# Performance work log

Hardware: AMD Instinct MI355X
Metric: run time of the kernel (lower is better)

Reference implementation:

```python
import jax, jax.numpy as jnp
import numpy as np

EPS = 1e-8  # torch cosine_similarity eps


def setup_inputs() -> dict:
    key = jax.random.key(0)
    kq, km = jax.random.split(key)
    B, N, D = 256, 100000, 1024
    query = jax.random.normal(kq, (B, D), dtype=jnp.float32)
    memory = jax.random.normal(km, (N, D), dtype=jnp.float32)
    return {"query": query, "memory": memory, "k": 16}


def reference(query, memory, k):
    # Batched, fused version of HierarchicalMemory.retrieve():
    # cosine similarity of each query against every stored module, then top-k.
    # sim(q, m) = q.m / max(||q||*||m||, eps), matching F.cosine_similarity.
    qn = jnp.linalg.norm(query, axis=-1)          # [B]
    mn = jnp.linalg.norm(memory, axis=-1)         # [N]
    dots = jnp.einsum("bd,nd->bn", query, memory)  # [B, N]
    sims = dots / jnp.maximum(qn[:, None] * mn[None, :], EPS)
    top_vals, top_idx = jax.lax.top_k(sims, k)    # [B, k] each
    return top_vals, top_idx
```

## Files before the change

### kernel.cpp

```cpp
#include <hip/hip_runtime.h>
#include <math.h>

#define DDIM 1024
#define BQ 256
#define EPSV 1e-8f
#define CH 4
#define TPC 32
#define NCAND (CH * TPC)

typedef short bf16x8 __attribute__((ext_vector_type(8)));
typedef float f32x4 __attribute__((ext_vector_type(4)));

__device__ __forceinline__ unsigned short f2bf(float x) {
  union { float f; unsigned int u; } v;
  v.f = x;
  unsigned int lsb = (v.u >> 16) & 1u;
  v.u += 0x7fffu + lsb;
  return (unsigned short)(v.u >> 16);
}
__device__ __forceinline__ float bf2f(unsigned short b) {
  union { unsigned int u; float f; } v;
  v.u = ((unsigned int)b) << 16;
  return v.f;
}

#define ASYNC_CP16(gp, lp)                                                     \
  __builtin_amdgcn_global_load_lds(                                            \
      (const __attribute__((address_space(1))) unsigned int*)(const void*)(gp),\
      (__attribute__((address_space(3))) unsigned int*)(lp), 16, 0, 0)

__global__ __launch_bounds__(256) void prep_q(const float* __restrict__ Q,
                                              unsigned short* __restrict__ Qb,
                                              float* __restrict__ qn) {
  int wave = threadIdx.x >> 6, lane = threadIdx.x & 63;
  int q = blockIdx.x * 4 + wave;
  const float4* src = (const float4*)(Q + (size_t)q * DDIM);
  unsigned short* dst = Qb + (size_t)q * DDIM;
  float s = 0.f;
#pragma unroll
  for (int t = 0; t < 4; ++t) {
    float4 v = src[t * 64 + lane];
    s += v.x * v.x + v.y * v.y + v.z * v.z + v.w * v.w;
    ushort4 o;
    o.x = f2bf(v.x); o.y = f2bf(v.y); o.z = f2bf(v.z); o.w = f2bf(v.w);
    *(ushort4*)(dst + t * 256 + lane * 4) = o;
  }
#pragma unroll
  for (int o = 32; o > 0; o >>= 1) s += __shfl_down(s, o, 64);
  if (lane == 0) qn[q] = sqrtf(s);
}

__global__ __launch_bounds__(256) void gemm_topk(
    const float* __restrict__ M, const unsigned short* __restrict__ Qb,
    unsigned short* __restrict__ sims, float* __restrict__ rmn,
    int N, int Npitch) {
  __shared__ unsigned short Qs[256 * 32];
  __shared__ unsigned short Ms[64 * 32];
  const int tid = threadIdx.x;
  const int wave = tid >> 6, lane = tid & 63;
  const int quad = lane >> 4, l15 = lane & 15;
  const int n0 = blockIdx.x * 64;

  const int mrow = tid >> 2;
  const int mchunk = tid & 3;
  const bool mvalid = (n0 + mrow) < N;
  const float* mptr = M + (size_t)(mvalid ? (n0 + mrow) : 0) * DDIM + mchunk * 8;

  f32x4 acc[4][4];
#pragma unroll
  for (int i = 0; i < 4; ++i)
#pragma unroll
    for (int j = 0; j < 4; ++j) acc[i][j] = (f32x4){0.f, 0.f, 0.f, 0.f};
  float sumsq = 0.f;

  for (int k0 = 0; k0 < DDIM; k0 += 32) {
    float4 m0, m1;
    if (mvalid) {
      m0 = *(const float4*)(mptr + k0);
      m1 = *(const float4*)(mptr + k0 + 4);
    } else {
      m0 = make_float4(0.f, 0.f, 0.f, 0.f);
      m1 = m0;
    }
    __syncthreads();
#pragma unroll
    for (int r = 0; r < 4; ++r) {
      int row0 = r * 64 + wave * 16;
      const unsigned short* g =
          Qb + (size_t)(row0 + (lane >> 2)) * DDIM + k0 + (lane & 3) * 8;
      ASYNC_CP16(g, &Qs[row0 * 32]);
    }
    sumsq += m0.x * m0.x + m0.y * m0.y + m0.z * m0.z + m0.w * m0.w +
             m1.x * m1.x + m1.y * m1.y + m1.z * m1.z + m1.w * m1.w;
    uint4 packed;
    packed.x = (unsigned int)f2bf(m0.x) | ((unsigned int)f2bf(m0.y) << 16);
    packed.y = (unsigned int)f2bf(m0.z) | ((unsigned int)f2bf(m0.w) << 16);
    packed.z = (unsigned int)f2bf(m1.x) | ((unsigned int)f2bf(m1.y) << 16);
    packed.w = (unsigned int)f2bf(m1.z) | ((unsigned int)f2bf(m1.w) << 16);
    *(uint4*)&Ms[mrow * 32 + mchunk * 8] = packed;
    __syncthreads();
    bf16x8 afr[4], bfr[4];
#pragma unroll
    for (int i = 0; i < 4; ++i)
      afr[i] = *(const bf16x8*)&Qs[(wave * 64 + i * 16 + l15) * 32 + quad * 8];
#pragma unroll
    for (int j = 0; j < 4; ++j)
      bfr[j] = *(const bf16x8*)&Ms[(j * 16 + l15) * 32 + quad * 8];
#pragma unroll
    for (int i = 0; i < 4; ++i)
#pragma unroll
      for (int j = 0; j < 4; ++j)
        acc[i][j] = __builtin_amdgcn_mfma_f32_16x16x32_bf16(afr[i], bfr[j],
                                                            acc[i][j], 0, 0, 0);
  }

  float s = sumsq;
  s += __shfl_xor(s, 1, 64);
  s += __shfl_xor(s, 2, 64);
  if (mchunk == 0) rmn[n0 + mrow] = (s > 0.f) ? rsqrtf(s) : 0.f;

#pragma unroll
  for (int i = 0; i < 4; ++i)
#pragma unroll
    for (int j = 0; j < 4; ++j)
#pragma unroll
      for (int r = 0; r < 4; ++r) {
        int q = wave * 64 + i * 16 + quad * 4 + r;
        int n = n0 + j * 16 + l15;
        sims[(size_t)q * Npitch + n] = f2bf(acc[i][j][r]);
      }
}

__device__ __forceinline__ bool better(float v1, int i1, float v2, int i2) {
  return v1 > v2 || (v1 == v2 && i1 < i2);
}

template <int L>
__device__ __forceinline__ void insert_topL(float (&tv)[L], int (&ti)[L],
                                            float v, int idx) {
  if (v > tv[L - 1] || (v == tv[L - 1] && idx < ti[L - 1])) {
    tv[L - 1] = v; ti[L - 1] = idx;
#pragma unroll
    for (int j = L - 1; j > 0; --j) {
      if (better(tv[j], ti[j], tv[j - 1], ti[j - 1])) {
        float fv = tv[j]; tv[j] = tv[j - 1]; tv[j - 1] = fv;
        int ii = ti[j]; ti[j] = ti[j - 1]; ti[j - 1] = ii;
      }
    }
  }
}

template <int L, typename F>
__device__ __forceinline__ void block_extract(float (&tv)[L], int (&ti)[L],
                                              int rounds, F&& emit) {
  __shared__ float s_v[4];
  __shared__ int s_i[4];
  __shared__ int s_t[4];
  __shared__ float s_wv;
  __shared__ int s_wi;
  __shared__ int s_wt;
  for (int r = 0; r < rounds; ++r) {
    float v = tv[0];
    int idx = ti[0];
    int src = threadIdx.x;
#pragma unroll
    for (int o = 32; o > 0; o >>= 1) {
      float ov = __shfl_down(v, o, 64);
      int oi = __shfl_down(idx, o, 64);
      int os = __shfl_down(src, o, 64);
      if (better(ov, oi, v, idx)) { v = ov; idx = oi; src = os; }
    }
    int lane = threadIdx.x & 63, w = threadIdx.x >> 6;
    if (lane == 0) { s_v[w] = v; s_i[w] = idx; s_t[w] = src; }
    __syncthreads();
    if (threadIdx.x == 0) {
      float bv = s_v[0]; int bi = s_i[0]; int bt = s_t[0];
      for (int w2 = 1; w2 < 4; ++w2)
        if (better(s_v[w2], s_i[w2], bv, bi)) { bv = s_v[w2]; bi = s_i[w2]; bt = s_t[w2]; }
      s_wv = bv; s_wi = bi; s_wt = bt;
    }
    __syncthreads();
    if (threadIdx.x == s_wt) {
#pragma unroll
      for (int j = 0; j < L - 1; ++j) { tv[j] = tv[j + 1]; ti[j] = ti[j + 1]; }
      tv[L - 1] = -INFINITY; ti[L - 1] = 0x7fffffff;
    }
    if (threadIdx.x == 0) emit(r, s_wv, s_wi);
    __syncthreads();
  }
}

__global__ __launch_bounds__(256) void select_chunks(
    const unsigned short* __restrict__ sims, const float* __restrict__ rmn,
    int* __restrict__ cand, int N, int Npitch, int Nc) {
  int q = blockIdx.y;
  int c = blockIdx.x;
  int start = c * Nc;
  int end = start + Nc;
  if (end > N) end = N;
  float tv[8]; int ti[8];
#pragma unroll
  for (int j = 0; j < 8; ++j) { tv[j] = -INFINITY; ti[j] = 0x7fffffff; }
  const unsigned short* row = sims + (size_t)q * Npitch;
  int base = start + threadIdx.x * 8;
  for (; base + 8 <= end; base += 2048) {
    uint4 wv = *(const uint4*)(row + base);
    float4 r0 = *(const float4*)&rmn[base];
    float4 r1 = *(const float4*)&rmn[base + 4];
    float f0 = bf2f((unsigned short)(wv.x & 0xffff)) * r0.x;
    float f1 = bf2f((unsigned short)(wv.x >> 16)) * r0.y;
    float f2 = bf2f((unsigned short)(wv.y & 0xffff)) * r0.z;
    float f3 = bf2f((unsigned short)(wv.y >> 16)) * r0.w;
    float f4 = bf2f((unsigned short)(wv.z & 0xffff)) * r1.x;
    float f5 = bf2f((unsigned short)(wv.z >> 16)) * r1.y;
    float f6 = bf2f((unsigned short)(wv.w & 0xffff)) * r1.z;
    float f7 = bf2f((unsigned short)(wv.w >> 16)) * r1.w;
    insert_topL<8>(tv, ti, f0, base + 0);
    insert_topL<8>(tv, ti, f1, base + 1);
    insert_topL<8>(tv, ti, f2, base + 2);
    insert_topL<8>(tv, ti, f3, base + 3);
    insert_topL<8>(tv, ti, f4, base + 4);
    insert_topL<8>(tv, ti, f5, base + 5);
    insert_topL<8>(tv, ti, f6, base + 6);
    insert_topL<8>(tv, ti, f7, base + 7);
  }
  if (base < end) {
    for (int n = base; n < end; ++n)
      insert_topL<8>(tv, ti, bf2f(row[n]) * rmn[n], n);
  }
  int* dst = cand + (size_t)q * NCAND + c * TPC;
  block_extract<8>(tv, ti, TPC, [&](int r, float v, int i) {
    dst[r] = (i == 0x7fffffff) ? 0 : i;
  });
}

__global__ __launch_bounds__(512) void rescore(
    const float* __restrict__ Q, const float* __restrict__ M,
    const float* __restrict__ qn, const int* __restrict__ cand,
    float* __restrict__ out, int N) {
  __shared__ float cosv[NCAND];
  __shared__ int cidx[NCAND];
  int q = blockIdx.x;
  int wave = threadIdx.x >> 6, lane = threadIdx.x & 63;
  const float4* qf4 = (const float4*)(Q + (size_t)q * DDIM);
  float4 qv[4];
#pragma unroll
  for (int t = 0; t < 4; ++t) qv[t] = qf4[t * 64 + lane];
  float qnv = qn[q];
#pragma unroll 1
  for (int i = 0; i < NCAND / 8; ++i) {
    int c = wave * (NCAND / 8) + i;
    int idx = cand[(size_t)q * NCAND + c];
    if (idx < 0 || idx >= N) idx = 0;
    const float4* mf4 = (const float4*)(M + (size_t)idx * DDIM);
    float dot = 0.f, sq = 0.f;
#pragma unroll
    for (int t = 0; t < 4; ++t) {
      float4 m = mf4[t * 64 + lane];
      dot += m.x * qv[t].x + m.y * qv[t].y + m.z * qv[t].z + m.w * qv[t].w;
      sq += m.x * m.x + m.y * m.y + m.z * m.z + m.w * m.w;
    }
#pragma unroll
    for (int o = 32; o > 0; o >>= 1) {
      dot += __shfl_down(dot, o, 64);
      sq += __shfl_down(sq, o, 64);
    }
    if (lane == 0) {
      cosv[c] = dot / fmaxf(qnv * sqrtf(sq), EPSV);
      cidx[c] = idx;
    }
  }
  __syncthreads();
  if (wave == 0) {
    float v0 = cosv[lane], v1 = cosv[lane + 64];
    int i0 = cidx[lane], i1 = cidx[lane + 64];
    for (int r = 0; r < 16; ++r) {
      bool fb = better(v0, i0, v1, i1);
      float bv = fb ? v0 : v1;
      int bi = fb ? i0 : i1;
      int bs = lane * 2 + (fb ? 0 : 1);
#pragma unroll
      for (int o = 32; o > 0; o >>= 1) {
        float ov = __shfl_down(bv, o, 64);
        int oi = __shfl_down(bi, o, 64);
        int os = __shfl_down(bs, o, 64);
        if (better(ov, oi, bv, bi)) { bv = ov; bi = oi; bs = os; }
      }
      bv = __shfl(bv, 0, 64);
      bi = __shfl(bi, 0, 64);
      bs = __shfl(bs, 0, 64);
      if (lane == (bs >> 1)) {
        if (bs & 1) v1 = -INFINITY; else v0 = -INFINITY;
      }
      if (lane == 0) {
        out[(size_t)q * 16 + r] = bv;
        out[(size_t)BQ * 16 + (size_t)q * 16 + r] = (float)bi;
      }
    }
  }
}

extern "C" void kernel_launch(void* const* d_in, const int* in_sizes, int n_in,
                              void* d_out, int out_size, void* d_ws, size_t ws_size,
                              hipStream_t stream) {
  const float* Q = (const float*)d_in[0];
  const float* M = (const float*)d_in[1];
  int N = in_sizes[1] / DDIM;
  float* out = (float*)d_out;

  int nb = (N + 63) / 64;
  int Npitch = nb * 64;

  char* w = (char*)d_ws;
  size_t off = 0;
  auto alloc = [&](size_t bytes) {
    char* p = w + off;
    off = (off + bytes + 255) & ~(size_t)255;
    return p;
  };
  unsigned short* Qb = (unsigned short*)alloc((size_t)BQ * DDIM * 2);
  float* qn = (float*)alloc((size_t)BQ * 4);
  float* rmn = (float*)alloc((size_t)Npitch * 4);
  int* cand = (int*)alloc((size_t)BQ * NCAND * 4);
  unsigned short* sims = (unsigned short*)alloc((size_t)BQ * Npitch * 2);
  (void)ws_size;

  int Nc = (((N + CH - 1) / CH) + 7) & ~7;

  prep_q<<<BQ / 4, 256, 0, stream>>>(Q, Qb, qn);
  gemm_topk<<<nb, 256, 0, stream>>>(M, Qb, sims, rmn, N, Npitch);
  select_chunks<<<dim3(CH, BQ), 256, 0, stream>>>(sims, rmn, cand, N, Npitch, Nc);
  rescore<<<BQ, 512, 0, stream>>>(Q, M, qn, cand, out, N);
}
```

Before: 745.5 us.

## Fold memory-norm scaling into GEMM epilogue, prefetch M, widen selection and rescore

The GEMM kernel now applies the reciprocal memory-row norm in its epilogue through shared memory, so the rmn buffer and its reads in the selection kernel go away. The fp32 memory loads are software-prefetched one k-step ahead to overlap global latency with MFMA work. Selection uses 8 chunks of 512 threads, each thread keeping a top-16 list, and emits 16 candidates per chunk. Rescoring processes two candidates per iteration to raise memory-level parallelism. The larger per-thread top-16 lists cost more registers and insertion work, and the tail loop in selection is now capped at 8 elements.

```diff
diff --git a/kernel.cpp b/kernel.cpp
--- a/kernel.cpp
+++ b/kernel.cpp
@@ -4,8 +4,8 @@
 #define DDIM 1024
 #define BQ 256
 #define EPSV 1e-8f
-#define CH 4
-#define TPC 32
+#define CH 8
+#define TPC 16
 #define NCAND (CH * TPC)
 
 typedef short bf16x8 __attribute__((ext_vector_type(8)));
@@ -52,10 +52,10 @@
 
 __global__ __launch_bounds__(256) void gemm_topk(
     const float* __restrict__ M, const unsigned short* __restrict__ Qb,
-    unsigned short* __restrict__ sims, float* __restrict__ rmn,
-    int N, int Npitch) {
+    unsigned short* __restrict__ sims, int N, int Npitch) {
   __shared__ unsigned short Qs[256 * 32];
   __shared__ unsigned short Ms[64 * 32];
+  __shared__ float Rs[64];
   const int tid = threadIdx.x;
   const int wave = tid >> 6, lane = tid & 63;
   const int quad = lane >> 4, l15 = lane & 15;
@@ -73,15 +73,13 @@
     for (int j = 0; j < 4; ++j) acc[i][j] = (f32x4){0.f, 0.f, 0.f, 0.f};
   float sumsq = 0.f;
 
+  float4 m0 = make_float4(0.f, 0.f, 0.f, 0.f), m1 = m0;
+  if (mvalid) {
+    m0 = *(const float4*)(mptr);
+    m1 = *(const float4*)(mptr + 4);
+  }
+
   for (int k0 = 0; k0 < DDIM; k0 += 32) {
-    float4 m0, m1;
-    if (mvalid) {
-      m0 = *(const float4*)(mptr + k0);
-      m1 = *(const float4*)(mptr + k0 + 4);
-    } else {
-      m0 = make_float4(0.f, 0.f, 0.f, 0.f);
-      m1 = m0;
-    }
     __syncthreads();
 #pragma unroll
     for (int r = 0; r < 4; ++r) {
@@ -99,6 +97,11 @@
     packed.w = (unsigned int)f2bf(m1.z) | ((unsigned int)f2bf(m1.w) << 16);
     *(uint4*)&Ms[mrow * 32 + mchunk * 8] = packed;
     __syncthreads();
+    float4 m0n = make_float4(0.f, 0.f, 0.f, 0.f), m1n = m0n;
+    if (k0 + 32 < DDIM && mvalid) {
+      m0n = *(const float4*)(mptr + k0 + 32);
+      m1n = *(const float4*)(mptr + k0 + 36);
+    }
     bf16x8 afr[4], bfr[4];
 #pragma unroll
     for (int i = 0; i < 4; ++i)
@@ -112,12 +115,18 @@
       for (int j = 0; j < 4; ++j)
         acc[i][j] = __builtin_amdgcn_mfma_f32_16x16x32_bf16(afr[i], bfr[j],
                                                             acc[i][j], 0, 0, 0);
+    m0 = m0n;
+    m1 = m1n;
   }
 
   float s = sumsq;
   s += __shfl_xor(s, 1, 64);
   s += __shfl_xor(s, 2, 64);
-  if (mchunk == 0) rmn[n0 + mrow] = (s > 0.f) ? rsqrtf(s) : 0.f;
+  if (mchunk == 0) Rs[mrow] = (s > 0.f) ? rsqrtf(s) : 0.f;
+  __syncthreads();
+  float rj[4];
+#pragma unroll
+  for (int j = 0; j < 4; ++j) rj[j] = Rs[j * 16 + l15];
 
 #pragma unroll
   for (int i = 0; i < 4; ++i)
@@ -127,7 +136,7 @@
       for (int r = 0; r < 4; ++r) {
         int q = wave * 64 + i * 16 + quad * 4 + r;
         int n = n0 + j * 16 + l15;
-        sims[(size_t)q * Npitch + n] = f2bf(acc[i][j][r]);
+        sims[(size_t)q * Npitch + n] = f2bf(acc[i][j][r] * rj[j]);
       }
 }
 
@@ -150,12 +159,12 @@
   }
 }
 
-template <int L, typename F>
+template <int L, int NW, typename F>
 __device__ __forceinline__ void block_extract(float (&tv)[L], int (&ti)[L],
                                               int rounds, F&& emit) {
-  __shared__ float s_v[4];
-  __shared__ int s_i[4];
-  __shared__ int s_t[4];
+  __shared__ float s_v[NW];
+  __shared__ int s_i[NW];
+  __shared__ int s_t[NW];
   __shared__ float s_wv;
   __shared__ int s_wi;
   __shared__ int s_wt;
@@ -175,7 +184,7 @@
     __syncthreads();
     if (threadIdx.x == 0) {
       float bv = s_v[0]; int bi = s_i[0]; int bt = s_t[0];
-      for (int w2 = 1; w2 < 4; ++w2)
+      for (int w2 = 1; w2 < NW; ++w2)
         if (better(s_v[w2], s_i[w2], bv, bi)) { bv = s_v[w2]; bi = s_i[w2]; bt = s_t[w2]; }
       s_wv = bv; s_wi = bi; s_wt = bt;
     }
@@ -190,46 +199,45 @@
   }
 }
 
-__global__ __launch_bounds__(256) void select_chunks(
-    const unsigned short* __restrict__ sims, const float* __restrict__ rmn,
-    int* __restrict__ cand, int N, int Npitch, int Nc) {
+__global__ __launch_bounds__(512) void select_chunks(
+    const unsigned short* __restrict__ sims, int* __restrict__ cand,
+    int N, int Npitch, int Nc) {
   int q = blockIdx.y;
   int c = blockIdx.x;
   int start = c * Nc;
   int end = start + Nc;
   if (end > N) end = N;
-  float tv[8]; int ti[8];
-#pragma unroll
-  for (int j = 0; j < 8; ++j) { tv[j] = -INFINITY; ti[j] = 0x7fffffff; }
+  float tv[16]; int ti[16];
+#pragma unroll
+  for (int j = 0; j < 16; ++j) { tv[j] = -INFINITY; ti[j] = 0x7fffffff; }
   const unsigned short* row = sims + (size_t)q * Npitch;
   int base = start + threadIdx.x * 8;
-  for (; base + 8 <= end; base += 2048) {
+  for (; base + 8 <= end; base += 4096) {
     uint4 wv = *(const uint4*)(row + base);
-    float4 r0 = *(const float4*)&rmn[base];
-    float4 r1 = *(const float4*)&rmn[base + 4];
-    float f0 = bf2f((unsigned short)(wv.x & 0xffff)) * r0.x;
-    float f1 = bf2f((unsigned short)(wv.x >> 16)) * r0.y;
-    float f2 = bf2f((unsigned short)(wv.y & 0xffff)) * r0.z;
-    float f3 = bf2f((unsigned short)(wv.y >> 16)) * r0.w;
-    float f4 = bf2f((unsigned short)(wv.z & 0xffff)) * r1.x;
-    float f5 = bf2f((unsigned short)(wv.z >> 16)) * r1.y;
-    float f6 = bf2f((unsigned short)(wv.w & 0xffff)) * r1.z;
-    float f7 = bf2f((unsigned short)(wv.w >> 16)) * r1.w;
-    insert_topL<8>(tv, ti, f0, base + 0);
-    insert_topL<8>(tv, ti, f1, base + 1);
-    insert_topL<8>(tv, ti, f2, base + 2);
-    insert_topL<8>(tv, ti, f3, base + 3);
-    insert_topL<8>(tv, ti, f4, base + 4);
-    insert_topL<8>(tv, ti, f5, base + 5);
-    insert_topL<8>(tv, ti, f6, base + 6);
-    insert_topL<8>(tv, ti, f7, base + 7);
+    float f0 = bf2f((unsigned short)(wv.x & 0xffff));
+    float f1 = bf2f((unsigned short)(wv.x >> 16));
+    float f2 = bf2f((unsigned short)(wv.y & 0xffff));
+    float f3 = bf2f((unsigned short)(wv.y >> 16));
+    float f4 = bf2f((unsigned short)(wv.z & 0xffff));
+    float f5 = bf2f((unsigned short)(wv.z >> 16));
+    float f6 = bf2f((unsigned short)(wv.w & 0xffff));
+    float f7 = bf2f((unsigned short)(wv.w >> 16));
+    insert_topL<16>(tv, ti, f0, base + 0);
+    insert_topL<16>(tv, ti, f1, base + 1);
+    insert_topL<16>(tv, ti, f2, base + 2);
+    insert_topL<16>(tv, ti, f3, base + 3);
+    insert_topL<16>(tv, ti, f4, base + 4);
+    insert_topL<16>(tv, ti, f5, base + 5);
+    insert_topL<16>(tv, ti, f6, base + 6);
+    insert_topL<16>(tv, ti, f7, base + 7);
   }
   if (base < end) {
-    for (int n = base; n < end; ++n)
-      insert_topL<8>(tv, ti, bf2f(row[n]) * rmn[n], n);
+    int stop = end - base < 8 ? end : base + 8;
+    for (int n = base; n < stop; ++n)
+      insert_topL<16>(tv, ti, bf2f(row[n]), n);
   }
   int* dst = cand + (size_t)q * NCAND + c * TPC;
-  block_extract<8>(tv, ti, TPC, [&](int r, float v, int i) {
+  block_extract<16, 8>(tv, ti, TPC, [&](int r, float v, int i) {
     dst[r] = (i == 0x7fffffff) ? 0 : i;
   });
 }
@@ -247,27 +255,39 @@
 #pragma unroll
   for (int t = 0; t < 4; ++t) qv[t] = qf4[t * 64 + lane];
   float qnv = qn[q];
+  const int per = NCAND / 8;
 #pragma unroll 1
-  for (int i = 0; i < NCAND / 8; ++i) {
-    int c = wave * (NCAND / 8) + i;
-    int idx = cand[(size_t)q * NCAND + c];
-    if (idx < 0 || idx >= N) idx = 0;
-    const float4* mf4 = (const float4*)(M + (size_t)idx * DDIM);
-    float dot = 0.f, sq = 0.f;
+  for (int i = 0; i < per; i += 2) {
+    int cA = wave * per + i;
+    int cB = cA + 1;
+    int idxA = cand[(size_t)q * NCAND + cA];
+    int idxB = cand[(size_t)q * NCAND + cB];
+    if (idxA < 0 || idxA >= N) idxA = 0;
+    if (idxB < 0 || idxB >= N) idxB = 0;
+    const float4* mA = (const float4*)(M + (size_t)idxA * DDIM);
+    const float4* mB = (const float4*)(M + (size_t)idxB * DDIM);
+    float dA = 0.f, sA = 0.f, dB = 0.f, sB = 0.f;
 #pragma unroll
     for (int t = 0; t < 4; ++t) {
-      float4 m = mf4[t * 64 + lane];
-      dot += m.x * qv[t].x + m.y * qv[t].y + m.z * qv[t].z + m.w * qv[t].w;
-      sq += m.x * m.x + m.y * m.y + m.z * m.z + m.w * m.w;
+      float4 a = mA[t * 64 + lane];
+      float4 b = mB[t * 64 + lane];
+      dA += a.x * qv[t].x + a.y * qv[t].y + a.z * qv[t].z + a.w * qv[t].w;
+      sA += a.x * a.x + a.y * a.y + a.z * a.z + a.w * a.w;
+      dB += b.x * qv[t].x + b.y * qv[t].y + b.z * qv[t].z + b.w * qv[t].w;
+      sB += b.x * b.x + b.y * b.y + b.z * b.z + b.w * b.w;
     }
 #pragma unroll
     for (int o = 32; o > 0; o >>= 1) {
-      dot += __shfl_down(dot, o, 64);
-      sq += __shfl_down(sq, o, 64);
+      dA += __shfl_down(dA, o, 64);
+      sA += __shfl_down(sA, o, 64);
+      dB += __shfl_down(dB, o, 64);
+      sB += __shfl_down(sB, o, 64);
     }
     if (lane == 0) {
-      cosv[c] = dot / fmaxf(qnv * sqrtf(sq), EPSV);
-      cidx[c] = idx;
+      cosv[cA] = dA / fmaxf(qnv * sqrtf(sA), EPSV);
+      cidx[cA] = idxA;
+      cosv[cB] = dB / fmaxf(qnv * sqrtf(sB), EPSV);
+      cidx[cB] = idxB;
     }
   }
   __syncthreads();
@@ -320,7 +340,6 @@
   };
   unsigned short* Qb = (unsigned short*)alloc((size_t)BQ * DDIM * 2);
   float* qn = (float*)alloc((size_t)BQ * 4);
-  float* rmn = (float*)alloc((size_t)Npitch * 4);
   int* cand = (int*)alloc((size_t)BQ * NCAND * 4);
   unsigned short* sims = (unsigned short*)alloc((size_t)BQ * Npitch * 2);
   (void)ws_size;
@@ -328,7 +347,7 @@
   int Nc = (((N + CH - 1) / CH) + 7) & ~7;
 
   prep_q<<<BQ / 4, 256, 0, stream>>>(Q, Qb, qn);
-  gemm_topk<<<nb, 256, 0, stream>>>(M, Qb, sims, rmn, N, Npitch);
-  select_chunks<<<dim3(CH, BQ), 256, 0, stream>>>(sims, rmn, cand, N, Npitch, Nc);
+  gemm_topk<<<nb, 256, 0, stream>>>(M, Qb, sims, N, Npitch);
+  select_chunks<<<dim3(CH, BQ), 512, 0, stream>>>(sims, cand, N, Npitch, Nc);
   rescore<<<BQ, 512, 0, stream>>>(Q, M, qn, cand, out, N);
 }
```

New measurement: 780.2 us. 4.7% more time.
